# Kernel tuning notes

Hardware: AMD Instinct MI355X
Metric: run time of the kernel (lower is better)

The kernel has to match this reference:

```python
import jax, jax.numpy as jnp
import numpy as np

NUM_HEADS = 16
NUM_GQA_GROUPS = 4
HEAD_DIM = 128
TOTAL_TOKENS = 4096
NUM_SEQS = 8
SCALE = HEAD_DIM ** -0.5


def setup_inputs() -> dict:
    key = jax.random.key(0)
    kq, kk, kv, kc = jax.random.split(key, 4)
    query = jax.random.normal(kq, (TOTAL_TOKENS, NUM_HEADS, HEAD_DIM), dtype=jnp.float32)
    k = jax.random.normal(kk, (TOTAL_TOKENS, NUM_GQA_GROUPS, HEAD_DIM), dtype=jnp.float32)
    v = jax.random.normal(kv, (TOTAL_TOKENS, NUM_GQA_GROUPS, HEAD_DIM), dtype=jnp.float32)
    # cu_seqlens: sorted prefix boundaries, pinned to 0 and TOTAL_TOKENS
    inner = jnp.sort(jax.random.randint(kc, (NUM_SEQS - 1,), 1, TOTAL_TOKENS, dtype=jnp.int32))
    cu_seqlens = jnp.concatenate([
        jnp.zeros((1,), jnp.int32), inner,
        jnp.full((1,), TOTAL_TOKENS, jnp.int32)])
    return {"query": query, "key": k, "value": v, "cu_seqlens": cu_seqlens}


def reference(query, key, value, cu_seqlens):
    """Packed varlen (thd) causal attention with GQA, fused via a segment mask.

    query: [T, H, D]; key/value: [T, G, D]; cu_seqlens: [B+1] int32.
    Returns [T, H, D] (same layout the torch thd path concatenates back to).
    """
    T, H, D = query.shape
    ratio = H // key.shape[1]
    if ratio > 1:  # GQA: repeat kv heads to match query heads
        key = jnp.repeat(key, ratio, axis=1)
        value = jnp.repeat(value, ratio, axis=1)

    pos = jnp.arange(T, dtype=jnp.int32)
    # segment id of each packed token: cu[j] <= i < cu[j+1]
    seg = jnp.searchsorted(cu_seqlens, pos, side="right") - 1
    # within-segment causal mask (global causal == local causal inside a segment)
    mask = (seg[:, None] == seg[None, :]) & (pos[:, None] >= pos[None, :])  # [T, T]

    scores = jnp.einsum("qhd,khd->hqk", query, key) * SCALE  # [H, T, T]
    scores = jnp.where(mask[None], scores, -jnp.inf)
    probs = jax.nn.softmax(scores, axis=-1)
    out = jnp.einsum("hqk,khd->qhd", probs, value)  # [T, H, D]
    return out
```

## Files before the change

### kernel.cpp

```cpp
#include <hip/hip_runtime.h>
#include <hip/hip_bf16.h>


#define T_TOK 4096
#define NH    16
#define NG    4
#define HD    128
#define NCU   9
#define NTILE 128

#define ML_OFF 33554432l
#define Q_OFF  (ML_OFF + 524288l)

typedef short          short8_t __attribute__((ext_vector_type(8)));
typedef float          float4_t __attribute__((ext_vector_type(4)));
typedef unsigned int   uint2_t  __attribute__((ext_vector_type(2)));
typedef unsigned short ushort;

static __device__ inline unsigned pack2(float a, float b) {
    __hip_bfloat162 h = __float22bfloat162_rn(make_float2(a, b));
    union { __hip_bfloat162 h; unsigned u; } c; c.h = h;
    return c.u;
}
static __device__ inline short8_t cvt8(float4_t lo, float4_t hi) {
    union { unsigned u[4]; short8_t s; } r;
    r.u[0] = pack2(lo[0], lo[1]); r.u[1] = pack2(lo[2], lo[3]);
    r.u[2] = pack2(hi[0], hi[1]); r.u[3] = pack2(hi[2], hi[3]);
    return r.s;
}

template <bool CHUNKED>
static __device__ __forceinline__ void attn_tile_body(
    const float* __restrict__ Q, const float* __restrict__ K,
    const float* __restrict__ V, const int* __restrict__ cu,
    float* __restrict__ O, float* __restrict__ WS,
    unsigned char* smem, int qtile, int g, int cz)
{
    ushort (*Ks)[32][136]   = (ushort (*)[32][136])smem;
    ushort (*Vt)[128][40]   = (ushort (*)[128][40])(smem + 17408);
    ushort (*pb)[2][16][40] = (ushort (*)[2][16][40])(smem + 37888);

    const int tid   = threadIdx.x;
    const int wave  = tid >> 6;
    const int split = wave >> 2;
    const int hw    = wave & 3;
    const int lane  = tid & 63;
    const int h     = g * 4 + hw;
    const int col   = lane & 15;
    const int quad  = lane >> 4;

    const int qbase = qtile * 32;
    const int qq[2] = { qbase + col, qbase + 16 + col };

    int seg_start[2] = {0, 0}, seg0 = 0;
    #pragma unroll
    for (int j = 1; j < NCU; ++j) {
        int cj = cu[j];
        if (cj <= qq[0])  seg_start[0] = cj;
        if (cj <= qq[1])  seg_start[1] = cj;
        if (cj <= qbase)  seg0         = cj;
    }
    const int k0       = seg0 & ~31;
    const int nblk_tot = (qbase + 32 - k0) >> 5;
    const int nc       = CHUNKED ? ((nblk_tot + 31) >> 5) : 1;
    if (CHUNKED && cz >= nc) return;
    int nblk = nblk_tot - (cz << 5);
    if (CHUNKED && nblk > 32) nblk = 32;
    const int nb0    = (nblk + 1) >> 1;
    const int kstart = k0 + (cz << 10) + split * nb0 * 32;

    short8_t qf[2][4];
    #pragma unroll
    for (int tt = 0; tt < 2; ++tt) {
        const float* qp = Q + ((long)qq[tt] * NH + h) * HD + quad * 8;
        #pragma unroll
        for (int c = 0; c < 4; ++c)
            qf[tt][c] = cvt8(*(const float4_t*)(qp + c * 32),
                             *(const float4_t*)(qp + c * 32 + 4));
    }

    float4_t oacc[2][8];
    #pragma unroll
    for (int tt = 0; tt < 2; ++tt)
        #pragma unroll
        for (int dt = 0; dt < 8; ++dt) oacc[tt][dt] = (float4_t){0.f, 0.f, 0.f, 0.f};

    float m_run[2] = {-10000.0f, -10000.0f};
    float l_run[2] = {0.0f, 0.0f};
    const float c_scale = 0.08838834764831845f * 1.4426950408889634f;

    const int stid = tid & 255;
    const int ki  = stid >> 3;
    const int ch  = (stid & 7) * 16;
    const int kp2 = (stid & 15) * 2;
    const int dc  = (stid >> 4) * 8;

    float4_t kreg[4], vreg[4];
    {
        int key = kstart + ki; if (key > T_TOK - 1) key = T_TOK - 1;
        const float* kp = K + ((long)key * NG + g) * HD + ch;
        kreg[0] = *(const float4_t*)kp;       kreg[1] = *(const float4_t*)(kp + 4);
        kreg[2] = *(const float4_t*)(kp + 8); kreg[3] = *(const float4_t*)(kp + 12);
        int key0 = kstart + kp2;     if (key0 > T_TOK - 1) key0 = T_TOK - 1;
        int key1 = kstart + kp2 + 1; if (key1 > T_TOK - 1) key1 = T_TOK - 1;
        const float* v0 = V + ((long)key0 * NG + g) * HD + dc;
        const float* v1 = V + ((long)key1 * NG + g) * HD + dc;
        vreg[0] = *(const float4_t*)v0; vreg[1] = *(const float4_t*)(v0 + 4);
        vreg[2] = *(const float4_t*)v1; vreg[3] = *(const float4_t*)(v1 + 4);
    }

    for (int it = 0; it < nb0; ++it) {
        const int kb = kstart + it * 32;
        __syncthreads();

        *(short8_t*)&Ks[split][ki][ch]     = cvt8(kreg[0], kreg[1]);
        *(short8_t*)&Ks[split][ki][ch + 8] = cvt8(kreg[2], kreg[3]);
        #pragma unroll
        for (int d = 0; d < 4; ++d) {
            *(unsigned*)&Vt[split][dc + d][kp2]     = pack2(vreg[0][d], vreg[2][d]);
            *(unsigned*)&Vt[split][dc + 4 + d][kp2] = pack2(vreg[1][d], vreg[3][d]);
        }
        __syncthreads();

        {
            int nb = kb + 32;
            int key = nb + ki; if (key > T_TOK - 1) key = T_TOK - 1;
            const float* kp = K + ((long)key * NG + g) * HD + ch;
            kreg[0] = *(const float4_t*)kp;       kreg[1] = *(const float4_t*)(kp + 4);
            kreg[2] = *(const float4_t*)(kp + 8); kreg[3] = *(const float4_t*)(kp + 12);
            int key0 = nb + kp2;     if (key0 > T_TOK - 1) key0 = T_TOK - 1;
            int key1 = nb + kp2 + 1; if (key1 > T_TOK - 1) key1 = T_TOK - 1;
            const float* v0 = V + ((long)key0 * NG + g) * HD + dc;
            const float* v1 = V + ((long)key1 * NG + g) * HD + dc;
            vreg[0] = *(const float4_t*)v0; vreg[1] = *(const float4_t*)(v0 + 4);
            vreg[2] = *(const float4_t*)v1; vreg[3] = *(const float4_t*)(v1 + 4);
        }

        float4_t st[2][2];
        #pragma unroll
        for (int tt = 0; tt < 2; ++tt)
            #pragma unroll
            for (int t = 0; t < 2; ++t) st[tt][t] = (float4_t){0.f, 0.f, 0.f, 0.f};
        #pragma unroll
        for (int c = 0; c < 4; ++c) {
            short8_t kf0 = *(const short8_t*)&Ks[split][col][c * 32 + quad * 8];
            short8_t kf1 = *(const short8_t*)&Ks[split][16 + col][c * 32 + quad * 8];
            st[0][0] = __builtin_amdgcn_mfma_f32_16x16x32_bf16(kf0, qf[0][c], st[0][0], 0, 0, 0);
            st[0][1] = __builtin_amdgcn_mfma_f32_16x16x32_bf16(kf1, qf[0][c], st[0][1], 0, 0, 0);
            st[1][0] = __builtin_amdgcn_mfma_f32_16x16x32_bf16(kf0, qf[1][c], st[1][0], 0, 0, 0);
            st[1][1] = __builtin_amdgcn_mfma_f32_16x16x32_bf16(kf1, qf[1][c], st[1][1], 0, 0, 0);
        }

        #pragma unroll
        for (int tt = 0; tt < 2; ++tt) {
            float tv[8];
            #pragma unroll
            for (int t = 0; t < 2; ++t)
                #pragma unroll
                for (int r = 0; r < 4; ++r) {
                    int key = kb + 16 * t + quad * 4 + r;
                    bool valid = (key <= qq[tt]) && (key >= seg_start[tt]);
                    tv[t * 4 + r] = valid ? st[tt][t][r] * c_scale : -30000.0f;
                }
            float tmax = tv[0];
            #pragma unroll
            for (int i = 1; i < 8; ++i) tmax = fmaxf(tmax, tv[i]);
            tmax = fmaxf(tmax, __shfl_xor(tmax, 16));
            tmax = fmaxf(tmax, __shfl_xor(tmax, 32));
            const float m_new = fmaxf(m_run[tt], tmax);
            float p[8], ps = 0.f;
            #pragma unroll
            for (int i = 0; i < 8; ++i) { p[i] = __builtin_exp2f(tv[i] - m_new); ps += p[i]; }
            ps += __shfl_xor(ps, 16);
            ps += __shfl_xor(ps, 32);
            if (__any(tmax > m_run[tt])) {
                const float alpha = __builtin_exp2f(m_run[tt] - m_new);
                l_run[tt] = l_run[tt] * alpha + ps;
                m_run[tt] = m_new;
                #pragma unroll
                for (int dt = 0; dt < 8; ++dt) oacc[tt][dt] *= alpha;
            } else {
                l_run[tt] += ps;
            }

            uint2_t w0; w0.x = pack2(p[0], p[1]); w0.y = pack2(p[2], p[3]);
            uint2_t w1; w1.x = pack2(p[4], p[5]); w1.y = pack2(p[6], p[7]);
            *(uint2_t*)&pb[wave][tt][col][quad * 4]      = w0;
            *(uint2_t*)&pb[wave][tt][col][16 + quad * 4] = w1;
        }
        short8_t pf0 = *(const short8_t*)&pb[wave][0][col][quad * 8];
        short8_t pf1 = *(const short8_t*)&pb[wave][1][col][quad * 8];

        #pragma unroll
        for (int dt = 0; dt < 8; ++dt) {
            short8_t vf = *(const short8_t*)&Vt[split][dt * 16 + col][quad * 8];
            oacc[0][dt] = __builtin_amdgcn_mfma_f32_16x16x32_bf16(vf, pf0, oacc[0][dt], 0, 0, 0);
            oacc[1][dt] = __builtin_amdgcn_mfma_f32_16x16x32_bf16(vf, pf1, oacc[1][dt], 0, 0, 0);
        }
    }

    float* Ob = (float*)smem;
    float* cm = (float*)(smem + 34816);
    float* cl = (float*)(smem + 35840);
    #pragma unroll
    for (int tt = 0; tt < 2; ++tt) {
        __syncthreads();
        if (split == 1) {
            if (quad == 0) { cm[hw * 16 + col] = m_run[tt]; cl[hw * 16 + col] = l_run[tt]; }
            float* ob = Ob + (hw * 16 + col) * 132;
            #pragma unroll
            for (int dt = 0; dt < 8; ++dt)
                *(float4_t*)(ob + dt * 16 + quad * 4) = oacc[tt][dt];
        }
        __syncthreads();
        if (split == 0) {
            const float m1 = cm[hw * 16 + col], l1 = cl[hw * 16 + col];
            const float m  = fmaxf(m_run[tt], m1);
            const float a0 = __builtin_exp2f(m_run[tt] - m);
            const float a1 = __builtin_exp2f(m1 - m);
            const float* ob = Ob + (hw * 16 + col) * 132;
            #pragma unroll
            for (int dt = 0; dt < 8; ++dt) {
                float4_t o1 = *(const float4_t*)(ob + dt * 16 + quad * 4);
                oacc[tt][dt] = oacc[tt][dt] * a0 + o1 * a1;
            }
            l_run[tt] = l_run[tt] * a0 + l1 * a1;
            m_run[tt] = m;
        }
    }

    if (split == 0) {
        if (!CHUNKED || nc == 1) {
            #pragma unroll
            for (int tt = 0; tt < 2; ++tt) {
                const float inv_l = 1.0f / l_run[tt];
                float* op = O + ((long)qq[tt] * NH + h) * HD + quad * 4;
                #pragma unroll
                for (int dt = 0; dt < 8; ++dt) {
                    float4_t ov;
                    #pragma unroll
                    for (int r = 0; r < 4; ++r) ov[r] = oacc[tt][dt][r] * inv_l;
                    *(float4_t*)(op + dt * 16) = ov;
                }
            }
        } else {
            const long slot = ((long)(qtile * 4 + g)) * 4 + cz;
            #pragma unroll
            for (int tt = 0; tt < 2; ++tt) {
                const int ql = tt * 16 + col;
                if (quad == 0) {
                    float* mlp = WS + ML_OFF + (slot * 128 + hw * 32 + ql) * 2;
                    mlp[0] = m_run[tt];
                    mlp[1] = l_run[tt];
                }
                float* op = WS + (slot * 128 + hw * 32 + ql) * 128 + quad * 4;
                #pragma unroll
                for (int dt = 0; dt < 8; ++dt)
                    *(float4_t*)(op + dt * 16) = oacc[tt][dt];
            }
        }
    }
}

__global__ __launch_bounds__(128) void build_queue(
    const int* __restrict__ cu, int* __restrict__ qwork)
{
    __shared__ int nblk_s[NTILE];
    __shared__ int sortedE[NTILE + 1];
    const int t = threadIdx.x;

    const int qbase = t * 32;
    int seg0 = 0;
    #pragma unroll
    for (int j = 1; j < NCU; ++j) { int cj = cu[j]; if (cj <= qbase) seg0 = cj; }
    const int k0   = seg0 & ~31;
    const int nblk = (qbase + 32 - k0) >> 5;
    nblk_s[t] = nblk;
    __syncthreads();

    int r = 0;
    for (int j = 0; j < NTILE; ++j) {
        int nj = nblk_s[j];
        if (nj > nblk || (nj == nblk && j < t)) ++r;
    }
    const int nc = (nblk + 31) >> 5;
    sortedE[r] = 4 * nc;
    __syncthreads();
    if (t == 0) {
        int s = 0;
        for (int j = 0; j < NTILE; ++j) { int v = sortedE[j]; sortedE[j] = s; s += v; }
        sortedE[NTILE] = s;
        qwork[0] = s;
        qwork[1] = 0;
    }
    __syncthreads();
    int off = 2 + sortedE[r];
    for (int g = 0; g < NG; ++g)
        for (int cz = 0; cz < nc; ++cz)
            qwork[off++] = (t << 4) | (g << 2) | cz;
}

__global__ __launch_bounds__(512) void attn_fwd_persist(
    const float* __restrict__ Q,
    const float* __restrict__ K,
    const float* __restrict__ V,
    const int*   __restrict__ cu,
    float*       __restrict__ O,
    float*       __restrict__ WS)
{
    __shared__ __align__(16) unsigned char smem[58368];
    __shared__ int pop_s;
    int* qwork = (int*)(WS + Q_OFF);
    const int qtotal = qwork[0];

    for (;;) {
        __syncthreads();
        if (threadIdx.x == 0) pop_s = atomicAdd(&qwork[1], 1);
        __syncthreads();
        const int idx = pop_s;
        if (idx >= qtotal) return;
        const int ent = qwork[2 + idx];
        attn_tile_body<true>(Q, K, V, cu, O, WS, smem,
                             ent >> 4, (ent >> 2) & 3, ent & 3);
    }
}

__global__ __launch_bounds__(512) void attn_fwd_mono(
    const float* __restrict__ Q,
    const float* __restrict__ K,
    const float* __restrict__ V,
    const int*   __restrict__ cu,
    float*       __restrict__ O)
{
    __shared__ __align__(16) unsigned char smem[58368];
    attn_tile_body<false>(Q, K, V, cu, O, nullptr, smem,
                          (int)gridDim.x - 1 - (int)blockIdx.x,
                          (int)blockIdx.y, 0);
}

__global__ __launch_bounds__(256) void attn_merge(
    const int*   __restrict__ cu,
    const float* __restrict__ WS,
    float*       __restrict__ O)
{
    const int tile  = blockIdx.x;
    const int g     = blockIdx.y;
    const int qbase = tile * 32;
    int seg0 = 0;
    #pragma unroll
    for (int j = 1; j < NCU; ++j) { int cj = cu[j]; if (cj <= qbase) seg0 = cj; }
    const int k0       = seg0 & ~31;
    const int nblk_tot = (qbase + 32 - k0) >> 5;
    const int nc       = (nblk_tot + 31) >> 5;
    if (nc <= 1) return;

    const int tid  = threadIdx.x;
    const int pair = tid >> 1;
    const int half = tid & 1;
    const int hw   = pair >> 5;
    const int q    = pair & 31;

    float m = -30000.0f, l = 0.0f;
    float4_t acc[16];
    #pragma unroll
    for (int i = 0; i < 16; ++i) acc[i] = (float4_t){0.f, 0.f, 0.f, 0.f};

    for (int c = 0; c < nc; ++c) {
        const long slot = ((long)(tile * 4 + g)) * 4 + c;
        const float* mlp = WS + ML_OFF + (slot * 128 + pair) * 2;
        const float mc = mlp[0], lc = mlp[1];
        const float mn = fmaxf(m, mc);
        const float a0 = __builtin_exp2f(m - mn);
        const float a1 = __builtin_exp2f(mc - mn);
        l = l * a0 + lc * a1;
        const float* op = WS + (slot * 128 + pair) * 128 + half * 64;
        #pragma unroll
        for (int i = 0; i < 16; ++i) {
            float4_t v = *(const float4_t*)(op + i * 4);
            acc[i] = acc[i] * a0 + v * a1;
        }
        m = mn;
    }
    const float inv = 1.0f / l;
    float* o = O + ((long)(qbase + q) * NH + g * 4 + hw) * HD + half * 64;
    #pragma unroll
    for (int i = 0; i < 16; ++i)
        *(float4_t*)(o + i * 4) = acc[i] * inv;
}

extern "C" void kernel_launch(void* const* d_in, const int* in_sizes, int n_in,
                              void* d_out, int out_size, void* d_ws, size_t ws_size,
                              hipStream_t stream) {
    const float* Q  = (const float*)d_in[0];
    const float* K  = (const float*)d_in[1];
    const float* V  = (const float*)d_in[2];
    const int*   cu = (const int*)d_in[3];
    float*       O  = (float*)d_out;
    const size_t need = (size_t)(33554432l + 524288l + 2056l) * sizeof(float);
    if (d_ws != nullptr && ws_size >= need) {
        float* WS = (float*)d_ws;
        build_queue<<<1, 128, 0, stream>>>(cu, (int*)(WS + Q_OFF));
        attn_fwd_persist<<<512, 512, 0, stream>>>(Q, K, V, cu, O, WS);
        attn_merge<<<dim3(T_TOK / 32, NG), 256, 0, stream>>>(
            cu, (const float*)WS, O);
    } else {
        attn_fwd_mono<<<dim3(T_TOK / 32, NG), 512, 0, stream>>>(Q, K, V, cu, O);
    }
}
```

Measured before the change: 188.2 us.

## Rebalance KV split-chunking across more chunks and skip masking on interior blocks

Changes the key-block chunking policy from fixed 32-block chunks to splitting each query tile into up to 4 roughly equal chunks once it has at least 8 blocks, applied consistently in the scheduler, the tile body and the merge kernel. This aims to cut load imbalance in the persistent work queue and improve parallelism for long sequences. It also adds a fast path that skips per-element causal/segment masking when a whole key block is fully valid for the row group. The cost is more partial results to write and merge.

```diff
diff --git a/kernel.cpp b/kernel.cpp
--- a/kernel.cpp
+++ b/kernel.cpp
@@ -27,6 +27,13 @@
     r.u[0] = pack2(lo[0], lo[1]); r.u[1] = pack2(lo[2], lo[3]);
     r.u[2] = pack2(hi[0], hi[1]); r.u[3] = pack2(hi[2], hi[3]);
     return r.s;
+}
+
+static __device__ __forceinline__ int nc_of(int nblk) {
+    int nc = nblk >> 3;
+    if (nc < 1) nc = 1;
+    if (nc > 4) nc = 4;
+    return nc;
 }
 
 template <bool CHUNKED>
@@ -62,12 +69,22 @@
     }
     const int k0       = seg0 & ~31;
     const int nblk_tot = (qbase + 32 - k0) >> 5;
-    const int nc       = CHUNKED ? ((nblk_tot + 31) >> 5) : 1;
-    if (CHUNKED && cz >= nc) return;
-    int nblk = nblk_tot - (cz << 5);
-    if (CHUNKED && nblk > 32) nblk = 32;
+
+    int nc, kb_lo, nblk;
+    if (CHUNKED) {
+        nc = nc_of(nblk_tot);
+        int chunk_kb = (nblk_tot + nc - 1) / nc;
+        chunk_kb = (chunk_kb + 1) & ~1;
+        kb_lo = cz * chunk_kb;
+        nblk  = nblk_tot - kb_lo;
+        if (nblk > chunk_kb) nblk = chunk_kb;
+    } else {
+        nc = 1; kb_lo = 0; nblk = nblk_tot;
+    }
     const int nb0    = (nblk + 1) >> 1;
-    const int kstart = k0 + (cz << 10) + split * nb0 * 32;
+    const int kstart = k0 + (kb_lo + split * nb0) * 32;
+
+    const int smax[2] = { __shfl(seg_start[0], 15), __shfl(seg_start[1], 15) };
 
     short8_t qf[2][4];
     #pragma unroll
@@ -154,14 +171,20 @@
         #pragma unroll
         for (int tt = 0; tt < 2; ++tt) {
             float tv[8];
-            #pragma unroll
-            for (int t = 0; t < 2; ++t)
+            if (kb + 31 <= qbase + 16 * tt && kb >= smax[tt]) {
                 #pragma unroll
-                for (int r = 0; r < 4; ++r) {
-                    int key = kb + 16 * t + quad * 4 + r;
-                    bool valid = (key <= qq[tt]) && (key >= seg_start[tt]);
-                    tv[t * 4 + r] = valid ? st[tt][t][r] * c_scale : -30000.0f;
-                }
+                for (int i = 0; i < 8; ++i)
+                    tv[i] = st[tt][i >> 2][i & 3] * c_scale;
+            } else {
+                #pragma unroll
+                for (int t = 0; t < 2; ++t)
+                    #pragma unroll
+                    for (int r = 0; r < 4; ++r) {
+                        int key = kb + 16 * t + quad * 4 + r;
+                        bool valid = (key <= qq[tt]) && (key >= seg_start[tt]);
+                        tv[t * 4 + r] = valid ? st[tt][t][r] * c_scale : -30000.0f;
+                    }
+            }
             float tmax = tv[0];
             #pragma unroll
             for (int i = 1; i < 8; ++i) tmax = fmaxf(tmax, tv[i]);
@@ -283,7 +306,7 @@
         int nj = nblk_s[j];
         if (nj > nblk || (nj == nblk && j < t)) ++r;
     }
-    const int nc = (nblk + 31) >> 5;
+    const int nc = nc_of(nblk);
     sortedE[r] = 4 * nc;
     __syncthreads();
     if (t == 0) {
@@ -351,7 +374,7 @@
     for (int j = 1; j < NCU; ++j) { int cj = cu[j]; if (cj <= qbase) seg0 = cj; }
     const int k0       = seg0 & ~31;
     const int nblk_tot = (qbase + 32 - k0) >> 5;
-    const int nc       = (nblk_tot + 31) >> 5;
+    const int nc       = nc_of(nblk_tot);
     if (nc <= 1) return;
 
     const int tid  = threadIdx.x;
```

Result: slower. 212.7 us (+13.0%).

## Double-buffer K/V LDS tiles, shuffle P in registers, skip masks on interior blocks

Applied to the files above, without the earlier changes.

K and V shared-memory tiles are now double-buffered by iteration parity, which removes one of the two block barriers per key block. The P matrix is moved between lanes with register shuffles instead of a round trip through LDS. Key blocks that lie entirely inside the causal and segment bounds skip the per-element mask compare. Shared memory grows to about 76 KB per block, which may lower occupancy, and the shuffle-based P layout must exactly match the old LDS layout.

```diff
diff --git a/kernel.cpp b/kernel.cpp
--- a/kernel.cpp
+++ b/kernel.cpp
@@ -14,7 +14,6 @@
 
 typedef short          short8_t __attribute__((ext_vector_type(8)));
 typedef float          float4_t __attribute__((ext_vector_type(4)));
-typedef unsigned int   uint2_t  __attribute__((ext_vector_type(2)));
 typedef unsigned short ushort;
 
 static __device__ inline unsigned pack2(float a, float b) {
@@ -36,9 +35,8 @@
     float* __restrict__ O, float* __restrict__ WS,
     unsigned char* smem, int qtile, int g, int cz)
 {
-    ushort (*Ks)[32][136]   = (ushort (*)[32][136])smem;
-    ushort (*Vt)[128][40]   = (ushort (*)[128][40])(smem + 17408);
-    ushort (*pb)[2][16][40] = (ushort (*)[2][16][40])(smem + 37888);
+    ushort (*Ks)[2][32][136] = (ushort (*)[2][32][136])smem;
+    ushort (*Vt)[2][128][42] = (ushort (*)[2][128][42])(smem + 34816);
 
     const int tid   = threadIdx.x;
     const int wave  = tid >> 6;
@@ -68,6 +66,8 @@
     if (CHUNKED && nblk > 32) nblk = 32;
     const int nb0    = (nblk + 1) >> 1;
     const int kstart = k0 + (cz << 10) + split * nb0 * 32;
+
+    const int smax[2] = { __shfl(seg_start[0], 15), __shfl(seg_start[1], 15) };
 
     short8_t qf[2][4];
     #pragma unroll
@@ -110,17 +110,16 @@
     }
 
     for (int it = 0; it < nb0; ++it) {
-        const int kb = kstart + it * 32;
-        __syncthreads();
-
-        *(short8_t*)&Ks[split][ki][ch]     = cvt8(kreg[0], kreg[1]);
-        *(short8_t*)&Ks[split][ki][ch + 8] = cvt8(kreg[2], kreg[3]);
+        const int kb  = kstart + it * 32;
+        const int buf = it & 1;
+
+        *(short8_t*)&Ks[buf][split][ki][ch]     = cvt8(kreg[0], kreg[1]);
+        *(short8_t*)&Ks[buf][split][ki][ch + 8] = cvt8(kreg[2], kreg[3]);
         #pragma unroll
         for (int d = 0; d < 4; ++d) {
-            *(unsigned*)&Vt[split][dc + d][kp2]     = pack2(vreg[0][d], vreg[2][d]);
-            *(unsigned*)&Vt[split][dc + 4 + d][kp2] = pack2(vreg[1][d], vreg[3][d]);
-        }
-        __syncthreads();
+            *(unsigned*)&Vt[buf][split][dc + d][kp2]     = pack2(vreg[0][d], vreg[2][d]);
+            *(unsigned*)&Vt[buf][split][dc + 4 + d][kp2] = pack2(vreg[1][d], vreg[3][d]);
+        }
 
         {
             int nb = kb + 32;
@@ -136,6 +135,8 @@
             vreg[2] = *(const float4_t*)v1; vreg[3] = *(const float4_t*)(v1 + 4);
         }
 
+        __syncthreads();
+
         float4_t st[2][2];
         #pragma unroll
         for (int tt = 0; tt < 2; ++tt)
@@ -143,25 +144,32 @@
             for (int t = 0; t < 2; ++t) st[tt][t] = (float4_t){0.f, 0.f, 0.f, 0.f};
         #pragma unroll
         for (int c = 0; c < 4; ++c) {
-            short8_t kf0 = *(const short8_t*)&Ks[split][col][c * 32 + quad * 8];
-            short8_t kf1 = *(const short8_t*)&Ks[split][16 + col][c * 32 + quad * 8];
+            short8_t kf0 = *(const short8_t*)&Ks[buf][split][col][c * 32 + quad * 8];
+            short8_t kf1 = *(const short8_t*)&Ks[buf][split][16 + col][c * 32 + quad * 8];
             st[0][0] = __builtin_amdgcn_mfma_f32_16x16x32_bf16(kf0, qf[0][c], st[0][0], 0, 0, 0);
             st[0][1] = __builtin_amdgcn_mfma_f32_16x16x32_bf16(kf1, qf[0][c], st[0][1], 0, 0, 0);
             st[1][0] = __builtin_amdgcn_mfma_f32_16x16x32_bf16(kf0, qf[1][c], st[1][0], 0, 0, 0);
             st[1][1] = __builtin_amdgcn_mfma_f32_16x16x32_bf16(kf1, qf[1][c], st[1][1], 0, 0, 0);
         }
 
+        short8_t pfv[2];
         #pragma unroll
         for (int tt = 0; tt < 2; ++tt) {
             float tv[8];
-            #pragma unroll
-            for (int t = 0; t < 2; ++t)
+            if (kb + 31 <= qbase + 16 * tt && kb >= smax[tt]) {
                 #pragma unroll
-                for (int r = 0; r < 4; ++r) {
-                    int key = kb + 16 * t + quad * 4 + r;
-                    bool valid = (key <= qq[tt]) && (key >= seg_start[tt]);
-                    tv[t * 4 + r] = valid ? st[tt][t][r] * c_scale : -30000.0f;
-                }
+                for (int i = 0; i < 8; ++i)
+                    tv[i] = st[tt][i >> 2][i & 3] * c_scale;
+            } else {
+                #pragma unroll
+                for (int t = 0; t < 2; ++t)
+                    #pragma unroll
+                    for (int r = 0; r < 4; ++r) {
+                        int key = kb + 16 * t + quad * 4 + r;
+                        bool valid = (key <= qq[tt]) && (key >= seg_start[tt]);
+                        tv[t * 4 + r] = valid ? st[tt][t][r] * c_scale : -30000.0f;
+                    }
+            }
             float tmax = tv[0];
             #pragma unroll
             for (int i = 1; i < 8; ++i) tmax = fmaxf(tmax, tv[i]);
@@ -183,19 +191,26 @@
                 l_run[tt] += ps;
             }
 
-            uint2_t w0; w0.x = pack2(p[0], p[1]); w0.y = pack2(p[2], p[3]);
-            uint2_t w1; w1.x = pack2(p[4], p[5]); w1.y = pack2(p[6], p[7]);
-            *(uint2_t*)&pb[wave][tt][col][quad * 4]      = w0;
-            *(uint2_t*)&pb[wave][tt][col][16 + quad * 4] = w1;
-        }
-        short8_t pf0 = *(const short8_t*)&pb[wave][0][col][quad * 8];
-        short8_t pf1 = *(const short8_t*)&pb[wave][1][col][quad * 8];
+            unsigned w0 = pack2(p[0], p[1]), w1 = pack2(p[2], p[3]);
+            unsigned w2 = pack2(p[4], p[5]), w3 = pack2(p[6], p[7]);
+            const int sl = col + 32 * (quad & 1);
+            union { unsigned u[4]; short8_t s; } pf;
+            unsigned a0 = __shfl(w0, sl),      b0 = __shfl(w2, sl);
+            unsigned a1 = __shfl(w1, sl),      b1 = __shfl(w3, sl);
+            unsigned a2 = __shfl(w0, sl + 16), b2 = __shfl(w2, sl + 16);
+            unsigned a3 = __shfl(w1, sl + 16), b3 = __shfl(w3, sl + 16);
+            pf.u[0] = (quad < 2) ? a0 : b0;
+            pf.u[1] = (quad < 2) ? a1 : b1;
+            pf.u[2] = (quad < 2) ? a2 : b2;
+            pf.u[3] = (quad < 2) ? a3 : b3;
+            pfv[tt] = pf.s;
+        }
 
         #pragma unroll
         for (int dt = 0; dt < 8; ++dt) {
-            short8_t vf = *(const short8_t*)&Vt[split][dt * 16 + col][quad * 8];
-            oacc[0][dt] = __builtin_amdgcn_mfma_f32_16x16x32_bf16(vf, pf0, oacc[0][dt], 0, 0, 0);
-            oacc[1][dt] = __builtin_amdgcn_mfma_f32_16x16x32_bf16(vf, pf1, oacc[1][dt], 0, 0, 0);
+            short8_t vf = *(const short8_t*)&Vt[buf][split][dt * 16 + col][quad * 8];
+            oacc[0][dt] = __builtin_amdgcn_mfma_f32_16x16x32_bf16(vf, pfv[0], oacc[0][dt], 0, 0, 0);
+            oacc[1][dt] = __builtin_amdgcn_mfma_f32_16x16x32_bf16(vf, pfv[1], oacc[1][dt], 0, 0, 0);
         }
     }
 
@@ -308,7 +323,7 @@
     float*       __restrict__ O,
     float*       __restrict__ WS)
 {
-    __shared__ __align__(16) unsigned char smem[58368];
+    __shared__ __align__(16) unsigned char smem[77824];
     __shared__ int pop_s;
     int* qwork = (int*)(WS + Q_OFF);
     const int qtotal = qwork[0];
@@ -332,7 +347,7 @@
     const int*   __restrict__ cu,
     float*       __restrict__ O)
 {
-    __shared__ __align__(16) unsigned char smem[58368];
+    __shared__ __align__(16) unsigned char smem[77824];
     attn_tile_body<false>(Q, K, V, cu, O, nullptr, smem,
                           (int)gridDim.x - 1 - (int)blockIdx.x,
                           (int)blockIdx.y, 0);
```

Result: slower. 208.7 us (+10.9%).

## Pre-convert Q/K/V to bf16 with transposed V, skip masking on interior blocks

Applied to the files above, without the earlier changes.

Adds a prep kernel that converts Q and K to bf16 and writes V as a transposed bf16 copy into workspace. The persistent attention kernel then loads these directly, cutting global traffic in half and removing the per-iteration conversion and the scattered transpose writes into shared memory. It also skips per-element causal and segment masking for key blocks that lie fully inside the valid region. The cost is an extra launch and an extra pass over the inputs. The new path only runs when the workspace is large enough, otherwise it falls back to the old paths.

```diff
diff --git a/kernel.cpp b/kernel.cpp
--- a/kernel.cpp
+++ b/kernel.cpp
@@ -9,8 +9,12 @@
 #define NCU   9
 #define NTILE 128
 
-#define ML_OFF 33554432l
-#define Q_OFF  (ML_OFF + 524288l)
+#define ML_OFF  33554432l
+#define Q_OFF   34078720l
+#define KBF_OFF 34080776l
+#define VTB_OFF 35129352l
+#define QBF_OFF 36177928l
+#define WS_END  40372232l
 
 typedef short          short8_t __attribute__((ext_vector_type(8)));
 typedef float          float4_t __attribute__((ext_vector_type(4)));
@@ -29,13 +33,65 @@
     return r.s;
 }
 
-template <bool CHUNKED>
+#define NPQ 4194304l
+#define NPK 1048576l
+__global__ __launch_bounds__(256) void prep_cvt(
+    const float* __restrict__ Q, const float* __restrict__ K,
+    const float* __restrict__ V, float* __restrict__ WS)
+{
+    unsigned* Qb  = (unsigned*)(WS + QBF_OFF);
+    unsigned* Kb  = (unsigned*)(WS + KBF_OFF);
+    ushort*   Vtb = (ushort*)(WS + VTB_OFF);
+    const int b = (int)blockIdx.x, tid = (int)threadIdx.x;
+    if (b < 2048) {
+        long p = (long)b * 256 + tid;
+        const long stride = 2048l * 256;
+        for (; p < NPQ + NPK; p += stride) {
+            if (p < NPQ) {
+                const float2 v = *(const float2*)&Q[2 * p];
+                Qb[p] = pack2(v.x, v.y);
+            } else {
+                const float2 v = *(const float2*)&K[2 * (p - NPQ)];
+                Kb[p - NPQ] = pack2(v.x, v.y);
+            }
+        }
+    } else {
+        const int bt  = b - 2048;
+        const int g   = bt >> 8;
+        const int rem = bt & 255;
+        const int d0  = (rem >> 6) * 32;
+        const int t0  = (rem & 63) * 64;
+        __shared__ ushort tile[64][36];
+        const int i2 = tid >> 3, jl = (tid & 7) * 4;
+        #pragma unroll
+        for (int ii = 0; ii < 2; ++ii) {
+            const int t = t0 + i2 + ii * 32;
+            const float4_t v = *(const float4_t*)&V[((long)t * NG + g) * HD + d0 + jl];
+            *(unsigned*)&tile[i2 + ii * 32][jl]     = pack2(v[0], v[1]);
+            *(unsigned*)&tile[i2 + ii * 32][jl + 2] = pack2(v[2], v[3]);
+        }
+        __syncthreads();
+        const int jj = tid >> 3, tl = (tid & 7) * 8;
+        union { ushort s[8]; short8_t v; } o;
+        #pragma unroll
+        for (int r = 0; r < 8; ++r) o.s[r] = tile[tl + r][jj];
+        *(short8_t*)&Vtb[((long)(g * HD + d0 + jj)) * T_TOK + t0 + tl] = o.v;
+    }
+}
+
+template <int MODE>
 static __device__ __forceinline__ void attn_tile_body(
     const float* __restrict__ Q, const float* __restrict__ K,
-    const float* __restrict__ V, const int* __restrict__ cu,
+    const float* __restrict__ V,
+    const ushort* __restrict__ Qb, const ushort* __restrict__ Kb,
+    const ushort* __restrict__ Vtb,
+    const int* __restrict__ cu,
     float* __restrict__ O, float* __restrict__ WS,
     unsigned char* smem, int qtile, int g, int cz)
 {
+    constexpr bool CHUNKED = (MODE >= 1);
+    constexpr bool BF      = (MODE == 2);
+
     ushort (*Ks)[32][136]   = (ushort (*)[32][136])smem;
     ushort (*Vt)[128][40]   = (ushort (*)[128][40])(smem + 17408);
     ushort (*pb)[2][16][40] = (ushort (*)[2][16][40])(smem + 37888);
@@ -69,14 +125,23 @@
     const int nb0    = (nblk + 1) >> 1;
     const int kstart = k0 + (cz << 10) + split * nb0 * 32;
 
+    const int smax[2] = { __shfl(seg_start[0], 15), __shfl(seg_start[1], 15) };
+
     short8_t qf[2][4];
     #pragma unroll
     for (int tt = 0; tt < 2; ++tt) {
-        const float* qp = Q + ((long)qq[tt] * NH + h) * HD + quad * 8;
-        #pragma unroll
-        for (int c = 0; c < 4; ++c)
-            qf[tt][c] = cvt8(*(const float4_t*)(qp + c * 32),
-                             *(const float4_t*)(qp + c * 32 + 4));
+        if constexpr (BF) {
+            const ushort* qp = Qb + ((long)qq[tt] * NH + h) * HD + quad * 8;
+            #pragma unroll
+            for (int c = 0; c < 4; ++c)
+                qf[tt][c] = *(const short8_t*)(qp + c * 32);
+        } else {
+            const float* qp = Q + ((long)qq[tt] * NH + h) * HD + quad * 8;
+            #pragma unroll
+            for (int c = 0; c < 4; ++c)
+                qf[tt][c] = cvt8(*(const float4_t*)(qp + c * 32),
+                                 *(const float4_t*)(qp + c * 32 + 4));
+        }
     }
 
     float4_t oacc[2][8];
@@ -94,9 +159,19 @@
     const int ch  = (stid & 7) * 16;
     const int kp2 = (stid & 15) * 2;
     const int dc  = (stid >> 4) * 8;
+    const int vd  = stid >> 1;
+    const int vko = (stid & 1) * 16;
 
     float4_t kreg[4], vreg[4];
-    {
+    short8_t krb[2], vrb[2];
+    if constexpr (BF) {
+        int key = kstart + ki; if (key > T_TOK - 1) key = T_TOK - 1;
+        const ushort* kp = Kb + ((long)key * NG + g) * HD + ch;
+        krb[0] = *(const short8_t*)kp; krb[1] = *(const short8_t*)(kp + 8);
+        int ts = kstart + vko; if (ts > T_TOK - 16) ts = T_TOK - 16;
+        const ushort* vp = Vtb + ((long)(g * HD + vd)) * T_TOK + ts;
+        vrb[0] = *(const short8_t*)vp; vrb[1] = *(const short8_t*)(vp + 8);
+    } else {
         int key = kstart + ki; if (key > T_TOK - 1) key = T_TOK - 1;
         const float* kp = K + ((long)key * NG + g) * HD + ch;
         kreg[0] = *(const float4_t*)kp;       kreg[1] = *(const float4_t*)(kp + 4);
@@ -113,27 +188,43 @@
         const int kb = kstart + it * 32;
         __syncthreads();
 
-        *(short8_t*)&Ks[split][ki][ch]     = cvt8(kreg[0], kreg[1]);
-        *(short8_t*)&Ks[split][ki][ch + 8] = cvt8(kreg[2], kreg[3]);
-        #pragma unroll
-        for (int d = 0; d < 4; ++d) {
-            *(unsigned*)&Vt[split][dc + d][kp2]     = pack2(vreg[0][d], vreg[2][d]);
-            *(unsigned*)&Vt[split][dc + 4 + d][kp2] = pack2(vreg[1][d], vreg[3][d]);
+        if constexpr (BF) {
+            *(short8_t*)&Ks[split][ki][ch]      = krb[0];
+            *(short8_t*)&Ks[split][ki][ch + 8]  = krb[1];
+            *(short8_t*)&Vt[split][vd][vko]     = vrb[0];
+            *(short8_t*)&Vt[split][vd][vko + 8] = vrb[1];
+        } else {
+            *(short8_t*)&Ks[split][ki][ch]     = cvt8(kreg[0], kreg[1]);
+            *(short8_t*)&Ks[split][ki][ch + 8] = cvt8(kreg[2], kreg[3]);
+            #pragma unroll
+            for (int d = 0; d < 4; ++d) {
+                *(unsigned*)&Vt[split][dc + d][kp2]     = pack2(vreg[0][d], vreg[2][d]);
+                *(unsigned*)&Vt[split][dc + 4 + d][kp2] = pack2(vreg[1][d], vreg[3][d]);
+            }
         }
         __syncthreads();
 
         {
             int nb = kb + 32;
-            int key = nb + ki; if (key > T_TOK - 1) key = T_TOK - 1;
-            const float* kp = K + ((long)key * NG + g) * HD + ch;
-            kreg[0] = *(const float4_t*)kp;       kreg[1] = *(const float4_t*)(kp + 4);
-            kreg[2] = *(const float4_t*)(kp + 8); kreg[3] = *(const float4_t*)(kp + 12);
-            int key0 = nb + kp2;     if (key0 > T_TOK - 1) key0 = T_TOK - 1;
-            int key1 = nb + kp2 + 1; if (key1 > T_TOK - 1) key1 = T_TOK - 1;
-            const float* v0 = V + ((long)key0 * NG + g) * HD + dc;
-            const float* v1 = V + ((long)key1 * NG + g) * HD + dc;
-            vreg[0] = *(const float4_t*)v0; vreg[1] = *(const float4_t*)(v0 + 4);
-            vreg[2] = *(const float4_t*)v1; vreg[3] = *(const float4_t*)(v1 + 4);
+            if constexpr (BF) {
+                int key = nb + ki; if (key > T_TOK - 1) key = T_TOK - 1;
+                const ushort* kp = Kb + ((long)key * NG + g) * HD + ch;
+                krb[0] = *(const short8_t*)kp; krb[1] = *(const short8_t*)(kp + 8);
+                int ts = nb + vko; if (ts > T_TOK - 16) ts = T_TOK - 16;
+                const ushort* vp = Vtb + ((long)(g * HD + vd)) * T_TOK + ts;
+                vrb[0] = *(const short8_t*)vp; vrb[1] = *(const short8_t*)(vp + 8);
+            } else {
+                int key = nb + ki; if (key > T_TOK - 1) key = T_TOK - 1;
+                const float* kp = K + ((long)key * NG + g) * HD + ch;
+                kreg[0] = *(const float4_t*)kp;       kreg[1] = *(const float4_t*)(kp + 4);
+                kreg[2] = *(const float4_t*)(kp + 8); kreg[3] = *(const float4_t*)(kp + 12);
+                int key0 = nb + kp2;     if (key0 > T_TOK - 1) key0 = T_TOK - 1;
+                int key1 = nb + kp2 + 1; if (key1 > T_TOK - 1) key1 = T_TOK - 1;
+                const float* v0 = V + ((long)key0 * NG + g) * HD + dc;
+                const float* v1 = V + ((long)key1 * NG + g) * HD + dc;
+                vreg[0] = *(const float4_t*)v0; vreg[1] = *(const float4_t*)(v0 + 4);
+                vreg[2] = *(const float4_t*)v1; vreg[3] = *(const float4_t*)(v1 + 4);
+            }
         }
 
         float4_t st[2][2];
@@ -154,14 +245,20 @@
         #pragma unroll
         for (int tt = 0; tt < 2; ++tt) {
             float tv[8];
-            #pragma unroll
-            for (int t = 0; t < 2; ++t)
+            if (kb + 31 <= qbase + 16 * tt && kb >= smax[tt]) {
                 #pragma unroll
-                for (int r = 0; r < 4; ++r) {
-                    int key = kb + 16 * t + quad * 4 + r;
-                    bool valid = (key <= qq[tt]) && (key >= seg_start[tt]);
-                    tv[t * 4 + r] = valid ? st[tt][t][r] * c_scale : -30000.0f;
-                }
+                for (int i = 0; i < 8; ++i)
+                    tv[i] = st[tt][i >> 2][i & 3] * c_scale;
+            } else {
+                #pragma unroll
+                for (int t = 0; t < 2; ++t)
+                    #pragma unroll
+                    for (int r = 0; r < 4; ++r) {
+                        int key = kb + 16 * t + quad * 4 + r;
+                        bool valid = (key <= qq[tt]) && (key >= seg_start[tt]);
+                        tv[t * 4 + r] = valid ? st[tt][t][r] * c_scale : -30000.0f;
+                    }
+            }
             float tmax = tv[0];
             #pragma unroll
             for (int i = 1; i < 8; ++i) tmax = fmaxf(tmax, tv[i]);
@@ -300,6 +397,7 @@
             qwork[off++] = (t << 4) | (g << 2) | cz;
 }
 
+template <int MODE>
 __global__ __launch_bounds__(512) void attn_fwd_persist(
     const float* __restrict__ Q,
     const float* __restrict__ K,
@@ -311,6 +409,9 @@
     __shared__ __align__(16) unsigned char smem[58368];
     __shared__ int pop_s;
     int* qwork = (int*)(WS + Q_OFF);
+    const ushort* Qb  = (const ushort*)(WS + QBF_OFF);
+    const ushort* Kb  = (const ushort*)(WS + KBF_OFF);
+    const ushort* Vtb = (const ushort*)(WS + VTB_OFF);
     const int qtotal = qwork[0];
 
     for (;;) {
@@ -320,7 +421,7 @@
         const int idx = pop_s;
         if (idx >= qtotal) return;
         const int ent = qwork[2 + idx];
-        attn_tile_body<true>(Q, K, V, cu, O, WS, smem,
+        attn_tile_body<MODE>(Q, K, V, Qb, Kb, Vtb, cu, O, WS, smem,
                              ent >> 4, (ent >> 2) & 3, ent & 3);
     }
 }
@@ -333,9 +434,9 @@
     float*       __restrict__ O)
 {
     __shared__ __align__(16) unsigned char smem[58368];
-    attn_tile_body<false>(Q, K, V, cu, O, nullptr, smem,
-                          (int)gridDim.x - 1 - (int)blockIdx.x,
-                          (int)blockIdx.y, 0);
+    attn_tile_body<0>(Q, K, V, nullptr, nullptr, nullptr, cu, O, nullptr, smem,
+                      (int)gridDim.x - 1 - (int)blockIdx.x,
+                      (int)blockIdx.y, 0);
 }
 
 __global__ __launch_bounds__(256) void attn_merge(
@@ -396,11 +497,19 @@
     const float* V  = (const float*)d_in[2];
     const int*   cu = (const int*)d_in[3];
     float*       O  = (float*)d_out;
-    const size_t need = (size_t)(33554432l + 524288l + 2056l) * sizeof(float);
-    if (d_ws != nullptr && ws_size >= need) {
+    const size_t need_bf  = (size_t)WS_END * sizeof(float);
+    const size_t need_f32 = (size_t)(33554432l + 524288l + 2056l) * sizeof(float);
+    if (d_ws != nullptr && ws_size >= need_bf) {
+        float* WS = (float*)d_ws;
+        prep_cvt<<<3072, 256, 0, stream>>>(Q, K, V, WS);
+        build_queue<<<1, 128, 0, stream>>>(cu, (int*)(WS + Q_OFF));
+        attn_fwd_persist<2><<<512, 512, 0, stream>>>(Q, K, V, cu, O, WS);
+        attn_merge<<<dim3(T_TOK / 32, NG), 256, 0, stream>>>(
+            cu, (const float*)WS, O);
+    } else if (d_ws != nullptr && ws_size >= need_f32) {
         float* WS = (float*)d_ws;
         build_queue<<<1, 128, 0, stream>>>(cu, (int*)(WS + Q_OFF));
-        attn_fwd_persist<<<512, 512, 0, stream>>>(Q, K, V, cu, O, WS);
+        attn_fwd_persist<1><<<512, 512, 0, stream>>>(Q, K, V, cu, O, WS);
         attn_merge<<<dim3(T_TOK / 32, NG), 256, 0, stream>>>(
             cu, (const float*)WS, O);
     } else {
```

Result: no change. 187.5 us (-0.4%).
